# Optimization experiments

Measured on AMD Instinct MI355X. Metric: run time of the kernel, lower is better.

The kernel has to match this reference:

```python
import jax, jax.numpy as jnp
import numpy as np

IN_FEATS, N_HIDDEN, N_CLASSES = 128, 256, 32
N0, N1, B = 614400, 40960, 4096
F0, F1 = 15, 10
BN_EPS = 1e-5


def setup_inputs() -> dict:
    key = jax.random.key(0)
    ks = jax.random.split(key, 20)
    s = 0.02
    inp = {
        "x": jax.random.uniform(ks[0], (N0, IN_FEATS), jnp.float32) * 10.0,
        "nbr0": jax.random.randint(ks[1], (N1, F0), 0, N0, jnp.int32),
        "nbr1": jax.random.randint(ks[2], (B, F1), 0, N1, jnp.int32),
        # layer0: SAGEConv(128->256, 'pool')
        "W_pool": jax.random.normal(ks[3], (IN_FEATS, IN_FEATS), jnp.float32) * s,
        "b_pool": jnp.zeros((IN_FEATS,), jnp.float32),
        "W_self0": jax.random.normal(ks[4], (N_HIDDEN, IN_FEATS), jnp.float32) * s,
        "W_neigh0": jax.random.normal(ks[5], (N_HIDDEN, IN_FEATS), jnp.float32) * s,
        "b0": jnp.zeros((N_HIDDEN,), jnp.float32),
        # BatchNorm1d(n_hidden)
        "gamma0": jnp.ones((N_HIDDEN,), jnp.float32),
        "beta0": jnp.zeros((N_HIDDEN,), jnp.float32),
        # layer1: SAGEConv(256->32, 'lstm'); torch LSTM gate order i,f,g,o
        "W_ih": jax.random.normal(ks[6], (4 * N_HIDDEN, N_HIDDEN), jnp.float32) * s,
        "W_hh": jax.random.normal(ks[7], (4 * N_HIDDEN, N_HIDDEN), jnp.float32) * s,
        "b_ih": jnp.zeros((4 * N_HIDDEN,), jnp.float32),
        "b_hh": jnp.zeros((4 * N_HIDDEN,), jnp.float32),
        "W_self1": jax.random.normal(ks[8], (N_CLASSES, N_HIDDEN), jnp.float32) * s,
        "W_neigh1": jax.random.normal(ks[9], (N_CLASSES, N_HIDDEN), jnp.float32) * s,
        "b1": jnp.zeros((N_CLASSES,), jnp.float32),
    }
    return inp


def _lstm_agg(seq, W_ih, W_hh, b_ih, b_hh):
    # seq: [B, K, H]; run LSTM over K neighbor steps, return final hidden [B, H]
    Bsz, _, H = seq.shape
    xs = jnp.swapaxes(seq, 0, 1)  # [K, B, H]

    def step(carry, x_t):
        h_t, c_t = carry
        g = x_t @ W_ih.T + b_ih + h_t @ W_hh.T + b_hh  # [B, 4H]
        i, f, gg, o = jnp.split(g, 4, axis=-1)
        c = jax.nn.sigmoid(f) * c_t + jax.nn.sigmoid(i) * jnp.tanh(gg)
        h = jax.nn.sigmoid(o) * jnp.tanh(c)
        return (h, c), None

    init = (jnp.zeros((Bsz, H), seq.dtype), jnp.zeros((Bsz, H), seq.dtype))
    (hT, _), _ = jax.lax.scan(step, init, xs)
    return hT


def reference(x, nbr0, nbr1, W_pool, b_pool, W_self0, W_neigh0, b0,
              gamma0, beta0, W_ih, W_hh, b_ih, b_hh, W_self1, W_neigh1, b1):
    n1 = nbr0.shape[0]
    b = nbr1.shape[0]
    h = jnp.log(x + 1.0)  # [N0, in_feats]

    # --- layer 0: SAGEConv 'pool' ---
    hp = jax.nn.relu(h @ W_pool.T + b_pool)           # [N0, in_feats]
    h_neigh = jnp.max(hp[nbr0], axis=1)               # [N1, in_feats]
    h0 = h[:n1] @ W_self0.T + h_neigh @ W_neigh0.T + b0  # [N1, n_hidden]

    # BN (training stats) + relu (dropout p=0)
    mu = jnp.mean(h0, axis=0)
    var = jnp.var(h0, axis=0)
    h0 = (h0 - mu) * jax.lax.rsqrt(var + BN_EPS) * gamma0 + beta0
    h0 = jax.nn.relu(h0)

    # --- layer 1: SAGEConv 'lstm' ---
    seq = h0[nbr1]                                    # [B, F1, n_hidden]
    h_neigh1 = _lstm_agg(seq, W_ih, W_hh, b_ih, b_hh)  # [B, n_hidden]
    out = h0[:b] @ W_self1.T + h_neigh1 @ W_neigh1.T + b1  # [B, n_classes]
    return out
```

## Files before the change

kernel.cpp:

```cpp
#include <hip/hip_runtime.h>

#define N0v 614400
#define N1v 40960
#define BATCHv 4096

typedef __attribute__((ext_vector_type(8))) short short8;
typedef __attribute__((ext_vector_type(4))) float floatx4;

static __device__ __forceinline__ float flog1p(float v) { return __logf(v + 1.0f); }
static __device__ __forceinline__ float sigf(float v) { return 1.0f / (1.0f + __expf(-v)); }
static __device__ __forceinline__ float tanhfast(float v) {
    return 1.0f - 2.0f / (__expf(2.0f * v) + 1.0f);
}
static __device__ __forceinline__ unsigned short f2bf(float f) {
    union { float f; unsigned u; } v; v.f = f;
    unsigned r = v.u + 0x7FFFu + ((v.u >> 16) & 1u);
    return (unsigned short)(r >> 16);
}
static __device__ __forceinline__ float bf2f(unsigned short u) {
    return __uint_as_float(((unsigned)u) << 16);
}

__global__ __launch_bounds__(256) void cvt_weights_kernel(
    const float* __restrict__ Wp, const float* __restrict__ Ws0,
    const float* __restrict__ Wn0, const float* __restrict__ Wih,
    const float* __restrict__ Whh, const float* __restrict__ bih,
    const float* __restrict__ bhh,
    unsigned short* __restrict__ Wpb, unsigned short* __restrict__ Ws0b,
    unsigned short* __restrict__ Wn0b, unsigned short* __restrict__ Wihb,
    unsigned short* __restrict__ Whhb, float* __restrict__ bsum)
{
    const int g = blockIdx.x * 256 + threadIdx.x;
    if (g < 16384)            Wpb[g] = f2bf(Wp[g]);
    else if (g < 49152)       Ws0b[g - 16384] = f2bf(Ws0[g - 16384]);
    else if (g < 81920)       Wn0b[g - 49152] = f2bf(Wn0[g - 49152]);
    else if (g < 344064)      Wihb[g - 81920] = f2bf(Wih[g - 81920]);
    else if (g < 606208)      Whhb[g - 344064] = f2bf(Whh[g - 344064]);
    else if (g < 607232) { const int i = g - 606208; bsum[i] = bih[i] + bhh[i]; }
}

__global__ __launch_bounds__(256) void pool_max_kernel(
    const float* __restrict__ x, const int* __restrict__ nbr0,
    const unsigned short* __restrict__ Wpb, const float* __restrict__ bp,
    unsigned short* __restrict__ hnb)
{
    __shared__ unsigned short smem[64 * 72 + 128 * 72];
    __shared__ unsigned red[512];
    __shared__ int nodes[64];
    unsigned short* aT = smem;
    unsigned short* wT = smem + 64 * 72;

    const int tid = threadIdx.x;
    const size_t base = (size_t)blockIdx.x * 60;
    if (tid < 64) nodes[tid] = (tid < 60) ? nbr0[base + tid] : 0;
    for (int i = tid; i < 512; i += 256) red[i] = 0u;

    const int lane = tid & 63, wv = tid >> 6;
    const int ml = lane & 15, q = lane >> 4, qk = q * 8;

    floatx4 acc[8];
#pragma unroll
    for (int ct = 0; ct < 8; ++ct) acc[ct] = (floatx4){0.f, 0.f, 0.f, 0.f};

    for (int kc = 0; kc < 2; ++kc) {
        __syncthreads();
        for (int i = tid; i < 512; i += 256) {
            const int row = i >> 3, seg = i & 7;
            short8 o = {0, 0, 0, 0, 0, 0, 0, 0};
            if (row < 60) {
                const float* s = x + (size_t)nodes[row] * 128 + kc * 64 + seg * 8;
                const float4 f0 = *(const float4*)s;
                const float4 f1 = *(const float4*)(s + 4);
                o[0] = (short)f2bf(flog1p(f0.x)); o[1] = (short)f2bf(flog1p(f0.y));
                o[2] = (short)f2bf(flog1p(f0.z)); o[3] = (short)f2bf(flog1p(f0.w));
                o[4] = (short)f2bf(flog1p(f1.x)); o[5] = (short)f2bf(flog1p(f1.y));
                o[6] = (short)f2bf(flog1p(f1.z)); o[7] = (short)f2bf(flog1p(f1.w));
            }
            *(short8*)&aT[row * 72 + seg * 8] = o;
        }
        for (int i = tid; i < 1024; i += 256) {
            const int row = i >> 3, seg = i & 7;
            *(short8*)&wT[row * 72 + seg * 8] =
                *(const short8*)&Wpb[(size_t)row * 128 + kc * 64 + seg * 8];
        }
        __syncthreads();
#pragma unroll
        for (int k0 = 0; k0 < 64; k0 += 32) {
            const short8 a = *(const short8*)&aT[(wv * 16 + ml) * 72 + k0 + qk];
#pragma unroll
            for (int ct = 0; ct < 8; ++ct) {
                const short8 b = *(const short8*)&wT[(ct * 16 + ml) * 72 + k0 + qk];
                acc[ct] = __builtin_amdgcn_mfma_f32_16x16x32_bf16(a, b, acc[ct], 0, 0, 0);
            }
        }
    }
    __syncthreads();
#pragma unroll
    for (int ct = 0; ct < 8; ++ct) {
        const int col = ct * 16 + ml;
        const float bb = bp[col];
#pragma unroll
        for (int r = 0; r < 4; ++r) {
            const int row = wv * 16 + q * 4 + r;
            if (row < 60) {
                const float v = fmaxf(acc[ct][r] + bb, 0.0f);
                atomicMax(&red[(row / 15) * 128 + col], __float_as_uint(v));
            }
        }
    }
    __syncthreads();
    for (int i = tid; i < 512; i += 256)
        hnb[(size_t)blockIdx.x * 512 + i] = f2bf(__uint_as_float(red[i]));
}

__global__ __launch_bounds__(256) void h0_kernel(
    const float* __restrict__ x, const unsigned short* __restrict__ hnb,
    const unsigned short* __restrict__ Ws0b, const unsigned short* __restrict__ Wn0b,
    const float* __restrict__ b0, unsigned short* __restrict__ h0bf,
    float* __restrict__ bn_sum, float* __restrict__ bn_sq)
{
    __shared__ unsigned short smem[64 * 72 + 128 * 72];
    unsigned short* aT = smem;
    unsigned short* wT = smem + 64 * 72;

    const int tid = threadIdx.x;
    const int m0 = blockIdx.x * 64, c0 = blockIdx.y * 128;
    const int lane = tid & 63, wv = tid >> 6;
    const int ml = lane & 15, q = lane >> 4, qk = q * 8;

    floatx4 acc[8];
#pragma unroll
    for (int ct = 0; ct < 8; ++ct) acc[ct] = (floatx4){0.f, 0.f, 0.f, 0.f};

    for (int kc = 0; kc < 4; ++kc) {
        __syncthreads();
        for (int i = tid; i < 512; i += 256) {
            const int row = i >> 3, seg = i & 7;
            const int k = kc * 64 + seg * 8;
            if (kc < 2) {
                const float* s = x + (size_t)(m0 + row) * 128 + k;
                const float4 f0 = *(const float4*)s;
                const float4 f1 = *(const float4*)(s + 4);
                short8 o;
                o[0] = (short)f2bf(flog1p(f0.x)); o[1] = (short)f2bf(flog1p(f0.y));
                o[2] = (short)f2bf(flog1p(f0.z)); o[3] = (short)f2bf(flog1p(f0.w));
                o[4] = (short)f2bf(flog1p(f1.x)); o[5] = (short)f2bf(flog1p(f1.y));
                o[6] = (short)f2bf(flog1p(f1.z)); o[7] = (short)f2bf(flog1p(f1.w));
                *(short8*)&aT[row * 72 + seg * 8] = o;
            } else {
                *(short8*)&aT[row * 72 + seg * 8] =
                    *(const short8*)&hnb[(size_t)(m0 + row) * 128 + (k - 128)];
            }
        }
        for (int i = tid; i < 1024; i += 256) {
            const int row = i >> 3, seg = i & 7;
            const int k = kc * 64 + seg * 8;
            const size_t cg = (size_t)(c0 + row);
            *(short8*)&wT[row * 72 + seg * 8] = (kc < 2)
                ? *(const short8*)&Ws0b[cg * 128 + k]
                : *(const short8*)&Wn0b[cg * 128 + (k - 128)];
        }
        __syncthreads();
#pragma unroll
        for (int k0 = 0; k0 < 64; k0 += 32) {
            const short8 a = *(const short8*)&aT[(wv * 16 + ml) * 72 + k0 + qk];
#pragma unroll
            for (int ct = 0; ct < 8; ++ct) {
                const short8 b = *(const short8*)&wT[(ct * 16 + ml) * 72 + k0 + qk];
                acc[ct] = __builtin_amdgcn_mfma_f32_16x16x32_bf16(a, b, acc[ct], 0, 0, 0);
            }
        }
    }
    __syncthreads();
    float* scr = (float*)smem;
#pragma unroll
    for (int ct = 0; ct < 8; ++ct) {
        const int col = ct * 16 + ml, cg = c0 + col;
        const float bb = b0[cg];
        float s = 0.f, sq = 0.f;
#pragma unroll
        for (int r = 0; r < 4; ++r) {
            const int row = wv * 16 + q * 4 + r;
            const float v = acc[ct][r] + bb;
            h0bf[(size_t)(m0 + row) * 256 + cg] = f2bf(v);
            s += v; sq += v * v;
        }
        scr[(wv * 4 + q) * 128 + col] = s;
        scr[2048 + (wv * 4 + q) * 128 + col] = sq;
    }
    __syncthreads();
    if (tid < 128) {
        float s = 0.f, sq = 0.f;
#pragma unroll
        for (int j = 0; j < 16; ++j) {
            s += scr[j * 128 + tid];
            sq += scr[2048 + j * 128 + tid];
        }
        atomicAdd(&bn_sum[c0 + tid], s);
        atomicAdd(&bn_sq[c0 + tid], sq);
    }
}

__global__ void bn_stats_kernel(const float* __restrict__ bn_sum, const float* __restrict__ bn_sq,
                                const float* __restrict__ gamma, const float* __restrict__ beta,
                                float* __restrict__ scale, float* __restrict__ shift)
{
    const int c = threadIdx.x;
    const float inv_n = 1.0f / (float)N1v;
    const float mu = bn_sum[c] * inv_n;
    const float var = bn_sq[c] * inv_n - mu * mu;
    const float rs = rsqrtf(var + 1e-5f);
    const float sc = rs * gamma[c];
    scale[c] = sc;
    shift[c] = beta[c] - mu * sc;
}

__global__ __launch_bounds__(256) void bn_apply_kernel(
    const unsigned short* __restrict__ h0bf, const float* __restrict__ scale,
    const float* __restrict__ shift, unsigned short* __restrict__ h0nbf)
{
    const int gid = blockIdx.x * 256 + threadIdx.x;
    const int c0 = (gid * 8) & 255;
    const short8 v = *(const short8*)&h0bf[(size_t)gid * 8];
    short8 o;
#pragma unroll
    for (int j = 0; j < 8; ++j) {
        const float f = bf2f((unsigned short)v[j]);
        o[j] = (short)f2bf(fmaxf(fmaf(f, scale[c0 + j], shift[c0 + j]), 0.0f));
    }
    *(short8*)&h0nbf[(size_t)gid * 8] = o;
}

__global__ __launch_bounds__(256) void lstm_gates_kernel(
    const unsigned short* __restrict__ h0nbf, const int* __restrict__ nbr1,
    const unsigned short* __restrict__ hbprev, const unsigned short* __restrict__ Wihb,
    const unsigned short* __restrict__ Whhb, const float* __restrict__ bsum,
    float* __restrict__ gbuf, int t)
{
    __shared__ unsigned short smem[64 * 72 + 128 * 72];
    __shared__ int nodes[64];
    unsigned short* aT = smem;
    unsigned short* wT = smem + 64 * 72;

    const int tid = threadIdx.x;
    const int m0 = blockIdx.x * 64, c0 = blockIdx.y * 128;
    const int lane = tid & 63, wv = tid >> 6;
    const int ml = lane & 15, q = lane >> 4, qk = q * 8;

    if (tid < 64) nodes[tid] = nbr1[(size_t)(m0 + tid) * 10 + t];

    floatx4 acc[8];
#pragma unroll
    for (int ct = 0; ct < 8; ++ct) acc[ct] = (floatx4){0.f, 0.f, 0.f, 0.f};

    for (int kc = 0; kc < 8; ++kc) {
        __syncthreads();
        for (int i = tid; i < 512; i += 256) {
            const int row = i >> 3, seg = i & 7;
            const int k = kc * 64 + seg * 8;
            *(short8*)&aT[row * 72 + seg * 8] = (kc < 4)
                ? *(const short8*)&h0nbf[(size_t)nodes[row] * 256 + k]
                : *(const short8*)&hbprev[(size_t)(m0 + row) * 256 + (k - 256)];
        }
        for (int i = tid; i < 1024; i += 256) {
            const int row = i >> 3, seg = i & 7;
            const int k = kc * 64 + seg * 8;
            const size_t cg = (size_t)(c0 + row);
            *(short8*)&wT[row * 72 + seg * 8] = (kc < 4)
                ? *(const short8*)&Wihb[cg * 256 + k]
                : *(const short8*)&Whhb[cg * 256 + (k - 256)];
        }
        __syncthreads();
#pragma unroll
        for (int k0 = 0; k0 < 64; k0 += 32) {
            const short8 a = *(const short8*)&aT[(wv * 16 + ml) * 72 + k0 + qk];
#pragma unroll
            for (int ct = 0; ct < 8; ++ct) {
                const short8 b = *(const short8*)&wT[(ct * 16 + ml) * 72 + k0 + qk];
                acc[ct] = __builtin_amdgcn_mfma_f32_16x16x32_bf16(a, b, acc[ct], 0, 0, 0);
            }
        }
    }
#pragma unroll
    for (int ct = 0; ct < 8; ++ct) {
        const int col = ct * 16 + ml;
        const float bb = bsum[c0 + col];
#pragma unroll
        for (int r = 0; r < 4; ++r) {
            const int row = wv * 16 + q * 4 + r;
            gbuf[(size_t)(m0 + row) * 1024 + c0 + col] = acc[ct][r] + bb;
        }
    }
}

__global__ __launch_bounds__(256) void lstm_point_kernel(
    const float* __restrict__ gbuf, float* __restrict__ cst,
    unsigned short* __restrict__ hb, int t)
{
    const int gid = blockIdx.x * 256 + threadIdx.x;
    const size_t b = (size_t)(gid >> 8);
    const int hh = gid & 255;
    const float gi = gbuf[b * 1024 + hh];
    const float gf = gbuf[b * 1024 + 256 + hh];
    const float gg = gbuf[b * 1024 + 512 + hh];
    const float go = gbuf[b * 1024 + 768 + hh];
    float c = sigf(gi) * tanhfast(gg);
    if (t > 0) c += sigf(gf) * cst[gid];
    cst[gid] = c;
    hb[gid] = f2bf(sigf(go) * tanhfast(c));
}

__global__ __launch_bounds__(256) void out_kernel(
    const unsigned short* __restrict__ h0nbf, const unsigned short* __restrict__ hTb,
    const float* __restrict__ Ws1, const float* __restrict__ Wn1,
    const float* __restrict__ b1, float* __restrict__ out)
{
    const int gid = blockIdx.x * 256 + threadIdx.x;
    const int row = gid >> 5, c = gid & 31;
    const unsigned short* a0 = h0nbf + (size_t)row * 256;
    const unsigned short* a1 = hTb + (size_t)row * 256;
    const float* w0 = Ws1 + (size_t)c * 256;
    const float* w1 = Wn1 + (size_t)c * 256;
    float s = b1[c];
#pragma unroll 4
    for (int k8 = 0; k8 < 32; ++k8) {
        const short8 av = *(const short8*)&a0[k8 * 8];
        const short8 bv = *(const short8*)&a1[k8 * 8];
        const float4 wa0 = *(const float4*)&w0[k8 * 8];
        const float4 wa1 = *(const float4*)&w0[k8 * 8 + 4];
        const float4 wb0 = *(const float4*)&w1[k8 * 8];
        const float4 wb1 = *(const float4*)&w1[k8 * 8 + 4];
        s += bf2f((unsigned short)av[0]) * wa0.x + bf2f((unsigned short)av[1]) * wa0.y;
        s += bf2f((unsigned short)av[2]) * wa0.z + bf2f((unsigned short)av[3]) * wa0.w;
        s += bf2f((unsigned short)av[4]) * wa1.x + bf2f((unsigned short)av[5]) * wa1.y;
        s += bf2f((unsigned short)av[6]) * wa1.z + bf2f((unsigned short)av[7]) * wa1.w;
        s += bf2f((unsigned short)bv[0]) * wb0.x + bf2f((unsigned short)bv[1]) * wb0.y;
        s += bf2f((unsigned short)bv[2]) * wb0.z + bf2f((unsigned short)bv[3]) * wb0.w;
        s += bf2f((unsigned short)bv[4]) * wb1.x + bf2f((unsigned short)bv[5]) * wb1.y;
        s += bf2f((unsigned short)bv[6]) * wb1.z + bf2f((unsigned short)bv[7]) * wb1.w;
    }
    out[gid] = s;
}

extern "C" void kernel_launch(void* const* d_in, const int* in_sizes, int n_in,
                              void* d_out, int out_size, void* d_ws, size_t ws_size,
                              hipStream_t stream)
{
    const float* x        = (const float*)d_in[0];
    const int*   nbr0     = (const int*)d_in[1];
    const int*   nbr1     = (const int*)d_in[2];
    const float* W_pool   = (const float*)d_in[3];
    const float* b_pool   = (const float*)d_in[4];
    const float* W_self0  = (const float*)d_in[5];
    const float* W_neigh0 = (const float*)d_in[6];
    const float* b0       = (const float*)d_in[7];
    const float* gamma0   = (const float*)d_in[8];
    const float* beta0    = (const float*)d_in[9];
    const float* W_ih     = (const float*)d_in[10];
    const float* W_hh     = (const float*)d_in[11];
    const float* b_ih     = (const float*)d_in[12];
    const float* b_hh     = (const float*)d_in[13];
    const float* W_self1  = (const float*)d_in[14];
    const float* W_neigh1 = (const float*)d_in[15];
    const float* b1       = (const float*)d_in[16];
    float* out = (float*)d_out;

    char* ws = (char*)d_ws;
    unsigned short* h0bf  = (unsigned short*)(ws);
    float*          gbuf  = (float*)(ws);
    unsigned short* hnb   = (unsigned short*)(ws + 20971520);
    unsigned short* h0nbf = (unsigned short*)(ws + 31457280);
    float*          cst   = (float*)(ws + 52428800);
    unsigned short* hb0   = (unsigned short*)(ws + 56623104);
    unsigned short* hb1   = (unsigned short*)(ws + 58720256);
    unsigned short* Wpb   = (unsigned short*)(ws + 60817408);
    unsigned short* Ws0b  = (unsigned short*)(ws + 60850176);
    unsigned short* Wn0b  = (unsigned short*)(ws + 60915712);
    unsigned short* Wihb  = (unsigned short*)(ws + 60981248);
    unsigned short* Whhb  = (unsigned short*)(ws + 61505536);
    float*          bsum  = (float*)(ws + 62029824);
    float*          bn_sum   = (float*)(ws + 62033920);
    float*          bn_sq    = (float*)(ws + 62034944);
    float*          bn_scale = (float*)(ws + 62035968);
    float*          bn_shift = (float*)(ws + 62036992);

    hipMemsetAsync(bn_sum, 0, 2048, stream);
    hipMemsetAsync(hb0, 0, 2097152, stream);

    cvt_weights_kernel<<<2372, 256, 0, stream>>>(W_pool, W_self0, W_neigh0, W_ih, W_hh,
                                                 b_ih, b_hh, Wpb, Ws0b, Wn0b, Wihb, Whhb, bsum);
    pool_max_kernel<<<N1v / 4, 256, 0, stream>>>(x, nbr0, Wpb, b_pool, hnb);
    h0_kernel<<<dim3(N1v / 64, 2), 256, 0, stream>>>(x, hnb, Ws0b, Wn0b, b0,
                                                     h0bf, bn_sum, bn_sq);
    bn_stats_kernel<<<1, 256, 0, stream>>>(bn_sum, bn_sq, gamma0, beta0, bn_scale, bn_shift);
    bn_apply_kernel<<<(N1v * 256 / 8) / 256, 256, 0, stream>>>(h0bf, bn_scale, bn_shift, h0nbf);

    for (int t = 0; t < 10; ++t) {
        const unsigned short* hp = (t & 1) ? hb1 : hb0;
        unsigned short*       hn = (t & 1) ? hb0 : hb1;
        lstm_gates_kernel<<<dim3(BATCHv / 64, 8), 256, 0, stream>>>(
            h0nbf, nbr1, hp, Wihb, Whhb, bsum, gbuf, t);
        lstm_point_kernel<<<BATCHv * 256 / 256, 256, 0, stream>>>(gbuf, cst, hn, t);
    }
    out_kernel<<<(BATCHv * 32) / 256, 256, 0, stream>>>(h0nbf, hb0, W_self1, W_neigh1, b1, out);
}
```

Measured before the change: 922.2 us.

## Fuse LSTM gate GEMM with pointwise cell update via gate-interleaved weight tiling

Each block now loads weight rows for the same 32 hidden units across all four gates (i,f,g,o), so it can apply the LSTM cell update straight from the MFMA accumulators. This removes the fp32 gate buffer write and re-read and the separate pointwise kernel launch on every timestep. The first step also skips the recurrent half of the K loop because h is zero, which removes the memset of the initial hidden state. The cost is more transcendental work in the GEMM epilogue and more scattered weight-row loads.

```diff
diff --git a/kernel.cpp b/kernel.cpp
--- a/kernel.cpp
+++ b/kernel.cpp
@@ -231,11 +231,11 @@
     *(short8*)&h0nbf[(size_t)gid * 8] = o;
 }
 
-__global__ __launch_bounds__(256) void lstm_gates_kernel(
+__global__ __launch_bounds__(256) void lstm_step_kernel(
     const unsigned short* __restrict__ h0nbf, const int* __restrict__ nbr1,
     const unsigned short* __restrict__ hbprev, const unsigned short* __restrict__ Wihb,
     const unsigned short* __restrict__ Whhb, const float* __restrict__ bsum,
-    float* __restrict__ gbuf, int t)
+    float* __restrict__ cst, unsigned short* __restrict__ hb, int t)
 {
     __shared__ unsigned short smem[64 * 72 + 128 * 72];
     __shared__ int nodes[64];
@@ -243,7 +243,7 @@
     unsigned short* wT = smem + 64 * 72;
 
     const int tid = threadIdx.x;
-    const int m0 = blockIdx.x * 64, c0 = blockIdx.y * 128;
+    const int m0 = blockIdx.x * 64, c0h = blockIdx.y * 32;
     const int lane = tid & 63, wv = tid >> 6;
     const int ml = lane & 15, q = lane >> 4, qk = q * 8;
 
@@ -253,7 +253,8 @@
 #pragma unroll
     for (int ct = 0; ct < 8; ++ct) acc[ct] = (floatx4){0.f, 0.f, 0.f, 0.f};
 
-    for (int kc = 0; kc < 8; ++kc) {
+    const int kcN = (t == 0) ? 4 : 8;
+    for (int kc = 0; kc < kcN; ++kc) {
         __syncthreads();
         for (int i = tid; i < 512; i += 256) {
             const int row = i >> 3, seg = i & 7;
@@ -265,10 +266,10 @@
         for (int i = tid; i < 1024; i += 256) {
             const int row = i >> 3, seg = i & 7;
             const int k = kc * 64 + seg * 8;
-            const size_t cg = (size_t)(c0 + row);
+            const size_t wr = (size_t)((row >> 5) * 256 + c0h + (row & 31));
             *(short8*)&wT[row * 72 + seg * 8] = (kc < 4)
-                ? *(const short8*)&Wihb[cg * 256 + k]
-                : *(const short8*)&Whhb[cg * 256 + (k - 256)];
+                ? *(const short8*)&Wihb[wr * 256 + k]
+                : *(const short8*)&Whhb[wr * 256 + (k - 256)];
         }
         __syncthreads();
 #pragma unroll
@@ -282,32 +283,26 @@
         }
     }
 #pragma unroll
-    for (int ct = 0; ct < 8; ++ct) {
-        const int col = ct * 16 + ml;
-        const float bb = bsum[c0 + col];
+    for (int hg = 0; hg < 2; ++hg) {
+        const int hcol = hg * 16 + ml;
+        const float bi = bsum[c0h + hcol];
+        const float bf_ = bsum[256 + c0h + hcol];
+        const float bg = bsum[512 + c0h + hcol];
+        const float bo = bsum[768 + c0h + hcol];
 #pragma unroll
         for (int r = 0; r < 4; ++r) {
             const int row = wv * 16 + q * 4 + r;
-            gbuf[(size_t)(m0 + row) * 1024 + c0 + col] = acc[ct][r] + bb;
-        }
-    }
-}
-
-__global__ __launch_bounds__(256) void lstm_point_kernel(
-    const float* __restrict__ gbuf, float* __restrict__ cst,
-    unsigned short* __restrict__ hb, int t)
-{
-    const int gid = blockIdx.x * 256 + threadIdx.x;
-    const size_t b = (size_t)(gid >> 8);
-    const int hh = gid & 255;
-    const float gi = gbuf[b * 1024 + hh];
-    const float gf = gbuf[b * 1024 + 256 + hh];
-    const float gg = gbuf[b * 1024 + 512 + hh];
-    const float go = gbuf[b * 1024 + 768 + hh];
-    float c = sigf(gi) * tanhfast(gg);
-    if (t > 0) c += sigf(gf) * cst[gid];
-    cst[gid] = c;
-    hb[gid] = f2bf(sigf(go) * tanhfast(c));
+            const size_t idx = (size_t)(m0 + row) * 256 + c0h + hcol;
+            const float gi = acc[hg][r] + bi;
+            const float gf = acc[2 + hg][r] + bf_;
+            const float gg = acc[4 + hg][r] + bg;
+            const float go = acc[6 + hg][r] + bo;
+            float c = sigf(gi) * tanhfast(gg);
+            if (t > 0) c += sigf(gf) * cst[idx];
+            cst[idx] = c;
+            hb[idx] = f2bf(sigf(go) * tanhfast(c));
+        }
+    }
 }
 
 __global__ __launch_bounds__(256) void out_kernel(
@@ -367,7 +362,6 @@
 
     char* ws = (char*)d_ws;
     unsigned short* h0bf  = (unsigned short*)(ws);
-    float*          gbuf  = (float*)(ws);
     unsigned short* hnb   = (unsigned short*)(ws + 20971520);
     unsigned short* h0nbf = (unsigned short*)(ws + 31457280);
     float*          cst   = (float*)(ws + 52428800);
@@ -385,7 +379,6 @@
     float*          bn_shift = (float*)(ws + 62036992);
 
     hipMemsetAsync(bn_sum, 0, 2048, stream);
-    hipMemsetAsync(hb0, 0, 2097152, stream);
 
     cvt_weights_kernel<<<2372, 256, 0, stream>>>(W_pool, W_self0, W_neigh0, W_ih, W_hh,
                                                  b_ih, b_hh, Wpb, Ws0b, Wn0b, Wihb, Whhb, bsum);
@@ -398,9 +391,8 @@
     for (int t = 0; t < 10; ++t) {
         const unsigned short* hp = (t & 1) ? hb1 : hb0;
         unsigned short*       hn = (t & 1) ? hb0 : hb1;
-        lstm_gates_kernel<<<dim3(BATCHv / 64, 8), 256, 0, stream>>>(
-            h0nbf, nbr1, hp, Wihb, Whhb, bsum, gbuf, t);
-        lstm_point_kernel<<<BATCHv * 256 / 256, 256, 0, stream>>>(gbuf, cst, hn, t);
+        lstm_step_kernel<<<dim3(BATCHv / 64, 8), 256, 0, stream>>>(
+            h0nbf, nbr1, hp, Wihb, Whhb, bsum, cst, hn, t);
     }
     out_kernel<<<(BATCHv * 32) / 256, 256, 0, stream>>>(h0nbf, hb0, W_self1, W_neigh1, b1, out);
 }
```

Result: faster. 777.1 us (-15.7%).
